# Kernel tuning notes

Measured on AMD Instinct MI355X. Metric: run time of the kernel, lower is better.

Reference implementation:

```python
import jax, jax.numpy as jnp
import numpy as np

HEADS = 16
DIM_HEAD = 64
QUERY_DIM = 1024
INNER = HEADS * DIM_HEAD


def setup_inputs() -> dict:
    key = jax.random.key(0)
    ks = jax.random.split(key, 6)
    b, n = 4, 2048
    s = 0.02
    return {
        "x": jax.random.normal(ks[0], (b, n, QUERY_DIM), dtype=jnp.float32),
        "Wq": jax.random.normal(ks[1], (QUERY_DIM, INNER), dtype=jnp.float32) * s,
        "Wk": jax.random.normal(ks[2], (QUERY_DIM, INNER), dtype=jnp.float32) * s,
        "Wv": jax.random.normal(ks[3], (QUERY_DIM, INNER), dtype=jnp.float32) * s,
        "Wo": jax.random.normal(ks[4], (INNER, QUERY_DIM), dtype=jnp.float32) * s,
        "bo": jax.random.normal(ks[5], (QUERY_DIM,), dtype=jnp.float32) * s,
    }


def reference(x, Wq, Wk, Wv, Wo, bo):
    b, n, _ = x.shape
    scale = DIM_HEAD ** (-0.5)
    # project and split heads: [b, n, inner] -> [b, h, n, d]
    def split(t):
        return t.reshape(b, n, HEADS, DIM_HEAD).transpose(0, 2, 1, 3)
    q = split(x @ Wq)
    k = split(x @ Wk)
    v = split(x @ Wv)
    sim = jnp.einsum('bhid,bhjd->bhij', q, k) * scale  # [b, h, n, n]
    attn = jax.nn.softmax(sim, axis=-1)
    out = jnp.einsum('bhij,bhjd->bhid', attn, v)  # [b, h, n, d]
    out = out.transpose(0, 2, 1, 3).reshape(b, n, INNER)
    return out @ Wo + bo
```

## Files before the change

### kernel.cpp

```cpp
#include <hip/hip_runtime.h>

typedef __attribute__((ext_vector_type(8))) short bf16x8;
typedef __attribute__((ext_vector_type(4))) float f32x4;
typedef __attribute__((ext_vector_type(16))) float f32x16;
typedef __attribute__((ext_vector_type(2))) unsigned u32x2;

__device__ __forceinline__ unsigned short f2b(float f) {
  union { float f; unsigned u; } x; x.f = f;
  unsigned r = x.u + 0x7fffu + ((x.u >> 16) & 1u);
  return (unsigned short)(r >> 16);
}

__device__ __forceinline__ int cvt_pk_bf16(float lo, float hi) {
  int r;
  asm("v_cvt_pk_bf16_f32 %0, %1, %2" : "=v"(r) : "v"(lo), "v"(hi));
  return r;
}

__device__ __forceinline__ float exp2_fast(float x) {
#if __has_builtin(__builtin_amdgcn_exp2f)
  return __builtin_amdgcn_exp2f(x);
#else
  return __expf(x * 0.69314718055994531f);
#endif
}

__device__ __forceinline__ void gl_lds16(const unsigned short* g, unsigned short* l) {
  __builtin_amdgcn_global_load_lds(
      (const __attribute__((address_space(1))) unsigned int*)(unsigned long long)g,
      (__attribute__((address_space(3))) unsigned int*)(unsigned)(unsigned long long)l,
      16, 0, 0);
}

#define MFMA(a, b, c) __builtin_amdgcn_mfma_f32_16x16x32_bf16((a), (b), (c), 0, 0, 0)
#define MFMA32(a, b, c) __builtin_amdgcn_mfma_f32_32x32x16_bf16((a), (b), (c), 0, 0, 0)

__global__ __launch_bounds__(256) void convert_x(const float* __restrict__ x,
                                                 unsigned short* __restrict__ xb) {
  int i = (blockIdx.x * 256 + threadIdx.x) * 4;
  float4 v = *(const float4*)(x + i);
  ushort4 o;
  o.x = f2b(v.x); o.y = f2b(v.y); o.z = f2b(v.z); o.w = f2b(v.w);
  *(ushort4*)(xb + i) = o;
}

__global__ __launch_bounds__(256) void transpose_w(const float* __restrict__ wq, const float* __restrict__ wk,
                                                   const float* __restrict__ wv, const float* __restrict__ wo,
                                                   unsigned short* __restrict__ tq, unsigned short* __restrict__ tk,
                                                   unsigned short* __restrict__ tv, unsigned short* __restrict__ to_) {
  int z = blockIdx.z;
  const float* W = (z == 0) ? wq : (z == 1) ? wk : (z == 2) ? wv : wo;
  unsigned short* T = (z == 0) ? tq : (z == 1) ? tk : (z == 2) ? tv : to_;
  float scale = (z == 0) ? 0.125f * 1.4426950408889634f : 1.0f;
  __shared__ float tile[64][65];
  int tr = blockIdx.y * 64, tc = blockIdx.x * 64;
  int t = threadIdx.x;
  int col = t & 63, r0 = (t >> 6) * 16;
#pragma unroll
  for (int r = 0; r < 16; r++)
    tile[r0 + r][col] = W[(long)(tr + r0 + r) * 1024 + tc + col];
  __syncthreads();
  int k = t & 63, n0 = (t >> 6) * 16;
#pragma unroll
  for (int n = 0; n < 16; n++)
    T[(long)(tc + n0 + n) * 1024 + tr + k] = f2b(tile[k][n0 + n] * scale);
}

__device__ __forceinline__ void gemm_core_256x128(const unsigned short* __restrict__ A,
                                                  const unsigned short* __restrict__ BT,
                                                  int m0, int n0,
                                                  unsigned short* As, unsigned short* Bs,
                                                  f32x4 acc[8][2]) {
  const int t = threadIdx.x;
  const int lane = t & 63;
  const int wid = t >> 6;
  const int wr = wid >> 2, wc = wid & 3;
  const int c = lane & 15, g = lane >> 4;

#define SA(hk, kt_, db)                                                                \
  {                                                                                    \
    _Pragma("unroll")                                                                  \
    for (int j = 0; j < 2; j++) {                                                      \
      int idx = j * 512 + t;                                                           \
      int row = idx >> 2, pl = idx & 3;                                                \
      int sc = (hk) * 4 + (pl ^ ((row >> 1) & 3));                                     \
      gl_lds16(A + (long)(m0 + row) * 1024 + (kt_) * 64 + sc * 8,                      \
               As + (db) * 16384 + (hk) * 8192 + idx * 8);                             \
    }                                                                                  \
  }
#define SB(hk, kt_, db)                                                                \
  {                                                                                    \
    int row = t >> 2, pl = t & 3;                                                      \
    int sc = (hk) * 4 + (pl ^ ((row >> 1) & 3));                                       \
    gl_lds16(BT + (long)(n0 + row) * 1024 + (kt_) * 64 + sc * 8,                       \
             Bs + (db) * 8192 + (hk) * 4096 + t * 8);                                  \
  }

#define RD_B(dstv, ks, buf)                                                            \
  {                                                                                    \
    _Pragma("unroll")                                                                  \
    for (int ni = 0; ni < 2; ni++) {                                                   \
      int row = wc * 32 + ni * 16 + c;                                                 \
      dstv[ni] = *(const bf16x8*)(Bs + (buf) * 8192 + (ks) * 4096 + row * 32 +         \
                                  ((g ^ ((row >> 1) & 3)) * 8));                       \
    }                                                                                  \
  }
#define RD_A(dstv, ks, qm, buf)                                                        \
  {                                                                                    \
    _Pragma("unroll")                                                                  \
    for (int i = 0; i < 4; i++) {                                                      \
      int row = wr * 128 + ((qm) * 4 + i) * 16 + c;                                    \
      dstv[i] = *(const bf16x8*)(As + (buf) * 16384 + (ks) * 8192 + row * 32 +         \
                                 ((g ^ ((row >> 1) & 3)) * 8));                        \
    }                                                                                  \
  }
#define DO_MFMA(afv, bfv, qm)                                                          \
  __builtin_amdgcn_s_setprio(1);                                                       \
  _Pragma("unroll")                                                                    \
  for (int i = 0; i < 4; i++)                                                          \
    _Pragma("unroll")                                                                  \
    for (int ni = 0; ni < 2; ni++)                                                     \
      acc[(qm) * 4 + i][ni] = MFMA(afv[i], bfv[ni], acc[(qm) * 4 + i][ni]);            \
  __builtin_amdgcn_s_setprio(0);

#define SYNC(n)                                                                        \
  asm volatile("s_waitcnt vmcnt(" #n ")" ::: "memory");                                \
  __builtin_amdgcn_s_barrier();                                                        \
  __builtin_amdgcn_sched_barrier(0);

  SA(0, 0, 0); SB(0, 0, 0); SA(1, 0, 0); SB(1, 0, 0);

  for (int kt = 0; kt < 16; kt++) {
    int buf = kt & 1, nb = buf ^ 1;
    bf16x8 af[4], bf[2];
    SYNC(3)
    RD_B(bf, 0, buf);
    RD_A(af, 0, 0, buf);
    if (kt < 15) SA(0, kt + 1, nb);
    DO_MFMA(af, bf, 0)
    RD_A(af, 0, 1, buf);
    if (kt < 15) SB(0, kt + 1, nb);
    DO_MFMA(af, bf, 1)
    if (kt < 15) { SYNC(3) } else { SYNC(0) }
    RD_B(bf, 1, buf);
    RD_A(af, 1, 0, buf);
    if (kt < 15) SA(1, kt + 1, nb);
    DO_MFMA(af, bf, 0)
    RD_A(af, 1, 1, buf);
    if (kt < 15) SB(1, kt + 1, nb);
    DO_MFMA(af, bf, 1)
  }
#undef SA
#undef SB
#undef RD_A
#undef RD_B
#undef DO_MFMA
#undef SYNC
}

__global__ __launch_bounds__(512) void gemm_qkv(const unsigned short* __restrict__ xb,
                                                const unsigned short* __restrict__ wtq,
                                                const unsigned short* __restrict__ wtk,
                                                const unsigned short* __restrict__ wtv,
                                                unsigned short* __restrict__ Qw,
                                                unsigned short* __restrict__ Kw,
                                                unsigned short* __restrict__ Vtw) {
  __shared__ unsigned short As[2 * 16384], Bs[2 * 8192];
  int m0 = blockIdx.x * 256;
  int nglob0 = blockIdx.y * 128;
  int which = nglob0 >> 10;
  const unsigned short* BT = (which == 0) ? wtq : (which == 1) ? wtk : wtv;
  int n0 = nglob0 & 1023;
  f32x4 acc[8][2] = {};
  gemm_core_256x128(xb, BT, m0, n0, As, Bs, acc);

  const int t = threadIdx.x;
  const int lane = t & 63, wid = t >> 6;
  const int wr = wid >> 2, wc = wid & 3;
  const int c = lane & 15, g = lane >> 4;
  int b = m0 >> 11;
  int ibase = m0 & 2047;
#pragma unroll
  for (int mi = 0; mi < 8; mi++) {
    int irow0 = ibase + wr * 128 + mi * 16 + g * 4;
#pragma unroll
    for (int ni = 0; ni < 2; ni++) {
      int nl = n0 + wc * 32 + ni * 16 + c;
      int h = nl >> 6, d = nl & 63;
      if (which == 2) {
        ushort4 pk;
        pk.x = f2b(acc[mi][ni][0]); pk.y = f2b(acc[mi][ni][1]);
        pk.z = f2b(acc[mi][ni][2]); pk.w = f2b(acc[mi][ni][3]);
        *(ushort4*)(Vtw + ((long)(b * 16 + h) * 64 + d) * 2048 + irow0) = pk;
      } else {
        unsigned short* dst = (which == 0) ? Qw : Kw;
#pragma unroll
        for (int r = 0; r < 4; r++)
          dst[((long)(b * 16 + h) * 2048 + irow0 + r) * 64 + d] = f2b(acc[mi][ni][r]);
      }
    }
  }
}

__global__ __launch_bounds__(512) void gemm_out(const unsigned short* __restrict__ Ao,
                                                const unsigned short* __restrict__ wto,
                                                const float* __restrict__ bias,
                                                float* __restrict__ out) {
  __shared__ unsigned short As[2 * 16384], Bs[2 * 8192];
  int m0 = blockIdx.x * 256;
  int n0 = blockIdx.y * 128;
  f32x4 acc[8][2] = {};
  gemm_core_256x128(Ao, wto, m0, n0, As, Bs, acc);

  const int t = threadIdx.x;
  const int lane = t & 63, wid = t >> 6;
  const int wr = wid >> 2, wc = wid & 3;
  const int c = lane & 15, g = lane >> 4;
#pragma unroll
  for (int mi = 0; mi < 8; mi++)
#pragma unroll
    for (int ni = 0; ni < 2; ni++) {
      int col = n0 + wc * 32 + ni * 16 + c;
      float bv = bias[col];
#pragma unroll
      for (int r = 0; r < 4; r++) {
        int row = m0 + wr * 128 + mi * 16 + g * 4 + r;
        out[(long)row * 1024 + col] = acc[mi][ni][r] + bv;
      }
    }
}

__global__ __launch_bounds__(512) void attn(const unsigned short* __restrict__ Qw,
                                            const unsigned short* __restrict__ Kw,
                                            const unsigned short* __restrict__ Vtw,
                                            unsigned short* __restrict__ Ow) {
  int ib = blockIdx.y * 8 + blockIdx.x;
  int xcd = ib & 7, j = ib >> 3;
  int bh = xcd * 8 + (j >> 3);
  int qt = j & 7;
  int t = threadIdx.x;
  int lane = t & 63, wid = t >> 6;
  int c5 = lane & 31, h = lane >> 5;
  __shared__ unsigned short Ks[2][64 * 64];
  __shared__ unsigned short Vs[2][64 * 64];

  const unsigned short* Qp = Qw + ((long)bh * 2048 + qt * 256 + wid * 32 + c5) * 64 + h * 8;
  bf16x8 qf[4];
#pragma unroll
  for (int dK = 0; dK < 4; dK++) qf[dK] = *(const bf16x8*)(Qp + dK * 16);

  f32x16 oacc0 = {}, oacc1 = {};
  float ls0 = 0.f, ls1 = 0.f, ls2 = 0.f, ls3 = 0.f;

  const unsigned short* Kbase = Kw + (long)bh * 2048 * 64;
  const unsigned short* Vbase = Vtw + (long)bh * 64 * 2048;

#define STAGE(jt_, buf_)                                                              \
  {                                                                                   \
    int row = t >> 3, ch = t & 7;                                                     \
    int sw = ch ^ (row & 7);                                                          \
    gl_lds16(Kbase + (long)((jt_) * 64 + row) * 64 + sw * 8, &Ks[buf_][t * 8]);       \
    gl_lds16(Vbase + (long)row * 2048 + (jt_) * 64 + sw * 8, &Vs[buf_][t * 8]);       \
  }

  STAGE(0, 0);

  union FR { int i[4]; bf16x8 v; };

  for (int jt = 0; jt < 32; jt++) {
    int buf = jt & 1;
    __syncthreads();
    if (jt + 1 < 32) STAGE(jt + 1, buf ^ 1);

    f32x16 s0 = {}, s1 = {};
#pragma unroll
    for (int dK = 0; dK < 4; dK++) {
      int sw = ((dK * 2 + h) ^ (c5 & 7)) * 8;
      bf16x8 k0 = *(const bf16x8*)(&Ks[buf][c5 * 64 + sw]);
      bf16x8 k1 = *(const bf16x8*)(&Ks[buf][c5 * 64 + sw + 2048]);
      s0 = MFMA32(k0, qf[dK], s0);
      s1 = MFMA32(k1, qf[dK], s1);
    }

    int pk[2][4][2];
#pragma unroll
    for (int q2 = 0; q2 < 4; q2++) {
      float a0 = exp2_fast(s0[q2 * 4 + 0]), a1 = exp2_fast(s0[q2 * 4 + 1]);
      float a2 = exp2_fast(s0[q2 * 4 + 2]), a3 = exp2_fast(s0[q2 * 4 + 3]);
      ls0 += a0 + a1; ls1 += a2 + a3;
      pk[0][q2][0] = cvt_pk_bf16(a0, a1);
      pk[0][q2][1] = cvt_pk_bf16(a2, a3);
      float b0 = exp2_fast(s1[q2 * 4 + 0]), b1 = exp2_fast(s1[q2 * 4 + 1]);
      float b2 = exp2_fast(s1[q2 * 4 + 2]), b3 = exp2_fast(s1[q2 * 4 + 3]);
      ls2 += b0 + b1; ls3 += b2 + b3;
      pk[1][q2][0] = cvt_pk_bf16(b0, b1);
      pk[1][q2][1] = cvt_pk_bf16(b2, b3);
    }

#pragma unroll
    for (int kblk = 0; kblk < 4; kblk++) {
      int kvb = kblk >> 1, e2c = (kblk & 1) * 2;
      u32x2 p0 = __builtin_amdgcn_permlane32_swap((unsigned)pk[kvb][e2c][0],
                                                  (unsigned)pk[kvb][e2c + 1][0], false, false);
      u32x2 p1 = __builtin_amdgcn_permlane32_swap((unsigned)pk[kvb][e2c][1],
                                                  (unsigned)pk[kvb][e2c + 1][1], false, false);
      FR fr;
      fr.i[0] = (int)p0[0];
      fr.i[1] = (int)p1[0];
      fr.i[2] = (int)p0[1];
      fr.i[3] = (int)p1[1];
      int sw = ((kblk * 2 + h) ^ (c5 & 7)) * 8;
      bf16x8 v0 = *(const bf16x8*)(&Vs[buf][c5 * 64 + sw]);
      bf16x8 v1 = *(const bf16x8*)(&Vs[buf][c5 * 64 + sw + 2048]);
      oacc0 = MFMA32(v0, fr.v, oacc0);
      oacc1 = MFMA32(v1, fr.v, oacc1);
    }
  }
#undef STAGE

  float lsum = ls0 + ls1 + ls2 + ls3;
  lsum += __shfl_xor(lsum, 32);
  float inv = 1.0f / lsum;
  int b = bh >> 4, hh = bh & 15;
  long row = (long)b * 2048 + qt * 256 + wid * 32 + c5;
  unsigned short* orow = Ow + row * 1024 + hh * 64;
#pragma unroll
  for (int dblk = 0; dblk < 2; dblk++) {
#pragma unroll
    for (int q2 = 0; q2 < 4; q2++) {
      float o0 = (dblk ? oacc1 : oacc0)[q2 * 4 + 0] * inv;
      float o1 = (dblk ? oacc1 : oacc0)[q2 * 4 + 1] * inv;
      float o2 = (dblk ? oacc1 : oacc0)[q2 * 4 + 2] * inv;
      float o3 = (dblk ? oacc1 : oacc0)[q2 * 4 + 3] * inv;
      ushort4 pkv;
      pkv.x = f2b(o0); pkv.y = f2b(o1); pkv.z = f2b(o2); pkv.w = f2b(o3);
      *(ushort4*)(orow + dblk * 32 + q2 * 8 + h * 4) = pkv;
    }
  }
}

extern "C" void kernel_launch(void* const* d_in, const int* in_sizes, int n_in,
                              void* d_out, int out_size, void* d_ws, size_t ws_size,
                              hipStream_t stream) {
  const float* x  = (const float*)d_in[0];
  const float* Wq = (const float*)d_in[1];
  const float* Wk = (const float*)d_in[2];
  const float* Wv = (const float*)d_in[3];
  const float* Wo = (const float*)d_in[4];
  const float* bo = (const float*)d_in[5];
  float* out = (float*)d_out;

  char* ws = (char*)d_ws;
  unsigned short* xb  = (unsigned short*)(ws);
  unsigned short* wtq = (unsigned short*)(ws + 16777216);
  unsigned short* wtk = (unsigned short*)(ws + 16777216 + 2097152);
  unsigned short* wtv = (unsigned short*)(ws + 16777216 + 2 * 2097152);
  unsigned short* wto = (unsigned short*)(ws + 16777216 + 3 * 2097152);
  unsigned short* Qw  = (unsigned short*)(ws + 25165824);
  unsigned short* Kw  = (unsigned short*)(ws + 25165824 + 16777216);
  unsigned short* Vtw = (unsigned short*)(ws + 25165824 + 2 * 16777216);
  unsigned short* Aow = xb;

  convert_x<<<8192, 256, 0, stream>>>(x, xb);
  transpose_w<<<dim3(16, 16, 4), 256, 0, stream>>>(Wq, Wk, Wv, Wo, wtq, wtk, wtv, wto);
  gemm_qkv<<<dim3(32, 24), 512, 0, stream>>>(xb, wtq, wtk, wtv, Qw, Kw, Vtw);
  attn<<<dim3(8, 64), 512, 0, stream>>>(Qw, Kw, Vtw, Aow);
  gemm_out<<<dim3(32, 8), 512, 0, stream>>>(Aow, wto, bo, out);
}
```

Baseline: 167.3 us.

## Triple-buffer K/V tiles in attention and merge prep kernels into one launch

The attention loop moves from double to triple buffering of K/V tiles in LDS. It prefetches two tiles ahead and replaces __syncthreads with an explicit vmcnt wait plus s_barrier, so global-to-LDS loads overlap more of the compute. Separately, convert_x and transpose_w are merged into a single prep kernel, removing one launch. The extra LDS raises per-block shared memory use, which may reduce occupancy. The hand-written waitcnt counts must match the number of outstanding loads issued per stage, and a miscount could cause a correctness race.

```diff
diff --git a/kernel.cpp b/kernel.cpp
--- a/kernel.cpp
+++ b/kernel.cpp
@@ -35,26 +35,30 @@
 #define MFMA(a, b, c) __builtin_amdgcn_mfma_f32_16x16x32_bf16((a), (b), (c), 0, 0, 0)
 #define MFMA32(a, b, c) __builtin_amdgcn_mfma_f32_32x32x16_bf16((a), (b), (c), 0, 0, 0)
 
-__global__ __launch_bounds__(256) void convert_x(const float* __restrict__ x,
-                                                 unsigned short* __restrict__ xb) {
-  int i = (blockIdx.x * 256 + threadIdx.x) * 4;
-  float4 v = *(const float4*)(x + i);
-  ushort4 o;
-  o.x = f2b(v.x); o.y = f2b(v.y); o.z = f2b(v.z); o.w = f2b(v.w);
-  *(ushort4*)(xb + i) = o;
-}
-
-__global__ __launch_bounds__(256) void transpose_w(const float* __restrict__ wq, const float* __restrict__ wk,
-                                                   const float* __restrict__ wv, const float* __restrict__ wo,
-                                                   unsigned short* __restrict__ tq, unsigned short* __restrict__ tk,
-                                                   unsigned short* __restrict__ tv, unsigned short* __restrict__ to_) {
-  int z = blockIdx.z;
+__global__ __launch_bounds__(256) void prep(const float* __restrict__ x, unsigned short* __restrict__ xb,
+                                            const float* __restrict__ wq, const float* __restrict__ wk,
+                                            const float* __restrict__ wv, const float* __restrict__ wo,
+                                            unsigned short* __restrict__ tq, unsigned short* __restrict__ tk,
+                                            unsigned short* __restrict__ tv, unsigned short* __restrict__ to_) {
+  int lin = blockIdx.x;
+  int t = threadIdx.x;
+  if (lin < 8192) {
+    int i = (lin * 256 + t) * 4;
+    float4 v = *(const float4*)(x + i);
+    ushort4 o;
+    o.x = f2b(v.x); o.y = f2b(v.y); o.z = f2b(v.z); o.w = f2b(v.w);
+    *(ushort4*)(xb + i) = o;
+    return;
+  }
+  int blk = lin - 8192;
+  int z = blk >> 8;
+  int rem = blk & 255;
+  int by = rem >> 4, bx = rem & 15;
   const float* W = (z == 0) ? wq : (z == 1) ? wk : (z == 2) ? wv : wo;
   unsigned short* T = (z == 0) ? tq : (z == 1) ? tk : (z == 2) ? tv : to_;
   float scale = (z == 0) ? 0.125f * 1.4426950408889634f : 1.0f;
   __shared__ float tile[64][65];
-  int tr = blockIdx.y * 64, tc = blockIdx.x * 64;
-  int t = threadIdx.x;
+  int tr = by * 64, tc = bx * 64;
   int col = t & 63, r0 = (t >> 6) * 16;
 #pragma unroll
   for (int r = 0; r < 16; r++)
@@ -241,8 +245,8 @@
   int t = threadIdx.x;
   int lane = t & 63, wid = t >> 6;
   int c5 = lane & 31, h = lane >> 5;
-  __shared__ unsigned short Ks[2][64 * 64];
-  __shared__ unsigned short Vs[2][64 * 64];
+  __shared__ unsigned short Ks[3][64 * 64];
+  __shared__ unsigned short Vs[3][64 * 64];
 
   const unsigned short* Qp = Qw + ((long)bh * 2048 + qt * 256 + wid * 32 + c5) * 64 + h * 8;
   bf16x8 qf[4];
@@ -264,13 +268,20 @@
   }
 
   STAGE(0, 0);
+  STAGE(1, 1);
 
   union FR { int i[4]; bf16x8 v; };
 
   for (int jt = 0; jt < 32; jt++) {
-    int buf = jt & 1;
-    __syncthreads();
-    if (jt + 1 < 32) STAGE(jt + 1, buf ^ 1);
+    int buf = jt % 3;
+    if (jt < 31) {
+      asm volatile("s_waitcnt vmcnt(2)" ::: "memory");
+    } else {
+      asm volatile("s_waitcnt vmcnt(0)" ::: "memory");
+    }
+    __builtin_amdgcn_s_barrier();
+    __builtin_amdgcn_sched_barrier(0);
+    if (jt + 2 < 32) STAGE(jt + 2, (jt + 2) % 3);
 
     f32x16 s0 = {}, s1 = {};
 #pragma unroll
@@ -361,8 +372,7 @@
   unsigned short* Vtw = (unsigned short*)(ws + 25165824 + 2 * 16777216);
   unsigned short* Aow = xb;
 
-  convert_x<<<8192, 256, 0, stream>>>(x, xb);
-  transpose_w<<<dim3(16, 16, 4), 256, 0, stream>>>(Wq, Wk, Wv, Wo, wtq, wtk, wtv, wto);
+  prep<<<9216, 256, 0, stream>>>(x, xb, Wq, Wk, Wv, Wo, wtq, wtk, wtv, wto);
   gemm_qkv<<<dim3(32, 24), 512, 0, stream>>>(xb, wtq, wtk, wtv, Qw, Kw, Vtw);
   attn<<<dim3(8, 64), 512, 0, stream>>>(Qw, Kw, Vtw, Aow);
   gemm_out<<<dim3(32, 8), 512, 0, stream>>>(Aow, wto, bo, out);
```

After: 166.2 us. About the same (-0.6%).
